# Optimization experiments

Measured on AMD Instinct MI355X. Metric: run time of the kernel, lower is better.

## Reference

```python
import jax, jax.numpy as jnp
import numpy as np

EPS_NORM = 1e-4
EPS_LOG = 1e-6


def normed_weight(W):
    # W: [O, I, K] (K=1). normalize() over dims (1,2) per output channel,
    # with norm scaled by alpha = sqrt(O / (O*I*K)) = 1/sqrt(I*K), then
    # divided again by sqrt(I*K) in get_normed_weight (eval path).
    O, I, K = W.shape
    fan_in = I * K
    norm = jnp.sqrt(jnp.sum(jnp.square(W), axis=(1, 2), keepdims=True))  # [O,1,1]
    norm = EPS_NORM + norm / np.sqrt(fan_in)
    return (W / norm) / np.sqrt(fan_in)


def complex_log(x):
    real = jnp.log(jnp.maximum(jnp.abs(x), EPS_LOG))
    imag = jnp.where(x < 0, jnp.pi, 0.0).astype(real.dtype)
    return jax.lax.complex(real, imag)


def logcumsumexp_complex(z, axis=-1):
    # stable complex logcumsumexp via associative scan:
    # logaddexp(a, b) = m + log(exp(a-m) + exp(b-m)), m = max(Re a, Re b)
    def combine(a, b):
        m = jnp.maximum(a.real, b.real)
        mc = jax.lax.complex(m, jnp.zeros_like(m))
        return mc + jnp.log(jnp.exp(a - mc) + jnp.exp(b - mc))
    return jax.lax.associative_scan(combine, z, axis=axis)


def min_gru(h, g):
    # h, g: [B, C, L]; parallel log-space minGRU recurrence along L
    log_scale = 0.5 * jnp.log(1.0 / jnp.cosh(g) + 1.0)
    log_coeffs = -jax.nn.softplus(g) + log_scale                 # real
    log_values = (-jax.nn.softplus(-g) + log_scale) + complex_log(h)  # complex
    a_star = jnp.cumsum(log_coeffs, axis=-1)                     # real
    a_star_c = jax.lax.complex(a_star, jnp.zeros_like(a_star))
    log_h = a_star_c + logcumsumexp_complex(log_values - a_star_c, axis=-1)
    return jnp.exp(log_h).real


def scaled_cat(xs, axis):
    Ns = [x.shape[axis] for x in xs]
    scale = np.sqrt(np.mean(Ns))
    return scale * jnp.concatenate([x * n ** -0.5 for n, x in zip(Ns, xs)], axis=axis)


def setup_inputs() -> dict:
    key = jax.random.key(0)
    k1, k2 = jax.random.split(key)
    B, D, L = 8, 512, 8192
    x = jax.random.normal(k1, (B, D, L), dtype=jnp.float32)
    W = jax.random.normal(k2, (2 * D, D, 1), dtype=jnp.float32)  # Conv1d(dim, 2*dim, 1) weight
    return {"x": x, "W": W}


def reference(x, W):
    Wn = normed_weight(W)  # [2D, D, 1]
    fb = jnp.einsum('oi,bil->bol', Wn[:, :, 0], x)  # [B, 2D, L]
    fore, back = jnp.split(fb, 2, axis=1)
    h_f, g_f = jnp.split(fore, 2, axis=1)
    back_r = back[..., ::-1]
    h_b, g_b = jnp.split(back_r, 2, axis=1)
    out_f = min_gru(h_f, g_f)
    out_b = min_gru(h_b, g_b)[..., ::-1]
    return scaled_cat([out_f, out_b], axis=1)
```

## Files before the change

kernel.cpp:

```cpp
#include <hip/hip_runtime.h>
#include <math.h>
#include <stdint.h>

#define LSEQ 8192
#define DIN  512
#define NB   8
#define NO   1024

typedef __bf16 bf16x8 __attribute__((ext_vector_type(8)));
typedef float f32x16 __attribute__((ext_vector_type(16)));

__device__ __forceinline__ uint32_t pack_bf16_rne(float lo, float hi) {
    uint32_t ul = __builtin_bit_cast(uint32_t, lo);
    uint32_t uh = __builtin_bit_cast(uint32_t, hi);
    ul += 0x7FFFu + ((ul >> 16) & 1u);
    uh += 0x7FFFu + ((uh >> 16) & 1u);
    return (ul >> 16) | (uh & 0xFFFF0000u);
}
__device__ __forceinline__ float bf16_lo(uint32_t w) {
    return __builtin_bit_cast(float, w << 16);
}
__device__ __forceinline__ float bf16_hi(uint32_t w) {
    return __builtin_bit_cast(float, w & 0xFFFF0000u);
}

__device__ __forceinline__ void gl_lds16(const void* g, void* l) {
    __builtin_amdgcn_global_load_lds(
        (const __attribute__((address_space(1))) void*)g,
        (__attribute__((address_space(3))) void*)l, 16, 0, 0);
}


__global__ void norm_kernel(const float* __restrict__ W, uint32_t* __restrict__ Wnb) {
    const int o = blockIdx.x;
    const int lane = threadIdx.x;
    const float* row = W + (size_t)o * DIN;
    float4 v0 = *(const float4*)(row + lane * 4);
    float4 v1 = *(const float4*)(row + 256 + lane * 4);
    float s = v0.x * v0.x + v0.y * v0.y + v0.z * v0.z + v0.w * v0.w
            + v1.x * v1.x + v1.y * v1.y + v1.z * v1.z + v1.w * v1.w;
#pragma unroll
    for (int m = 32; m; m >>= 1) s += __shfl_xor(s, m, 64);
    const float sq = 22.62741699796952f;
    const float scale = 1.0f / ((1e-4f + sqrtf(s) / sq) * sq);
    uint2 w0, w1;
    w0.x = pack_bf16_rne(v0.x * scale, v0.y * scale);
    w0.y = pack_bf16_rne(v0.z * scale, v0.w * scale);
    w1.x = pack_bf16_rne(v1.x * scale, v1.y * scale);
    w1.y = pack_bf16_rne(v1.z * scale, v1.w * scale);
    const int ot = o >> 7, mb = (o >> 5) & 3, m31 = o & 31;
    const int it0 = lane >> 3;
    const int q   = (lane >> 1) & 3;
    const int wic = (lane & 1) * 2;
    uint32_t* base = Wnb + (size_t)ot * 32768 + ((mb * 4 + q) * 32 + m31) * 4 + wic;
    *(uint2*)&base[(size_t)it0 * 2048] = w0;
    *(uint2*)&base[(size_t)(it0 + 8) * 2048] = w1;
}

__global__ __launch_bounds__(256)
void xpack_kernel(const float* __restrict__ x, uint32_t* __restrict__ xp) {
    __shared__ uint32_t sT[32 * 132];
    const int t  = threadIdx.x;
    const int bx = blockIdx.x;
    const int b  = blockIdx.y;
    const int lt = bx >> 3;
    const int ch = bx & 7;

    const float* xb = x + (size_t)b * DIN * LSEQ + lt * 128;
#pragma unroll
    for (int j = 0; j < 4; ++j) {
        const int idx = j * 256 + t;
        const int k2l = idx >> 5;
        const int lg  = idx & 31;
        const float* r0 = xb + (size_t)(2 * (ch * 32 + k2l)) * LSEQ + lg * 4;
        float4 a = *(const float4*)r0;
        float4 c = *(const float4*)(r0 + LSEQ);
        uint4 wv;
        wv.x = pack_bf16_rne(a.x, c.x);
        wv.y = pack_bf16_rne(a.y, c.y);
        wv.z = pack_bf16_rne(a.z, c.z);
        wv.w = pack_bf16_rne(a.w, c.w);
        *(uint4*)&sT[k2l * 132 + lg * 4] = wv;
    }
    __syncthreads();
    uint32_t* ob = xp + (size_t)(b * 64 + lt) * 32768;
#pragma unroll
    for (int j = 0; j < 4; ++j) {
        const int idx = j * 256 + t;
        const int lp  = idx >> 3;
        const int gq  = idx & 7;
        uint4 wv;
        wv.x = sT[(gq * 4 + 0) * 132 + lp];
        wv.y = sT[(gq * 4 + 1) * 132 + lp];
        wv.z = sT[(gq * 4 + 2) * 132 + lp];
        wv.w = sT[(gq * 4 + 3) * 132 + lp];
        const int itl   = ch * 2 + (gq >> 2);
        const int q     = gq & 3;
        const int chunk = ((lp >> 5) * 4 + q) * 32 + (lp & 31);
        *(uint4*)&ob[(size_t)itl * 2048 + chunk * 4] = wv;
    }
}

__global__ __launch_bounds__(256)
void gemm_kernel(const uint32_t* __restrict__ Wnb, const uint32_t* __restrict__ xp,
                 uint32_t* __restrict__ fbp) {
    __shared__ uint32_t sA[2][2048];
    __shared__ uint32_t sB[2][2048];

    const int tid  = threadIdx.x;
    const int lane = tid & 63;
    const int w    = tid >> 6;
    const int wm   = w & 1, wn = w >> 1;

    const int bx  = blockIdx.x;
    const int xcd = bx & 7;
    const int t   = bx >> 3;
    const int o0t = t & 7;
    const int o0  = o0t * 128;
    const int ltg = xcd + ((t >> 3) << 3);
    const int l0  = ltg * 128;
    const int b   = blockIdx.y;

    const uint32_t* gA = Wnb + (size_t)o0t * 32768 + (w * 2) * 256 + lane * 4;
    const uint32_t* gB = xp + (size_t)(b * 64 + ltg) * 32768 + (w * 2) * 256 + lane * 4;

    f32x16 acc[2][2];
#pragma unroll
    for (int i = 0; i < 2; ++i)
#pragma unroll
        for (int j = 0; j < 2; ++j)
#pragma unroll
            for (int r = 0; r < 16; ++r) acc[i][j][r] = 0.f;

#define STAGE(it, bs)                                               \
    do {                                                            \
        gl_lds16(gA + (size_t)(it) * 2048, &sA[bs][w * 512]);       \
        gl_lds16(gA + (size_t)(it) * 2048 + 256, &sA[bs][w * 512 + 256]); \
        gl_lds16(gB + (size_t)(it) * 2048, &sB[bs][w * 512]);       \
        gl_lds16(gB + (size_t)(it) * 2048 + 256, &sB[bs][w * 512 + 256]); \
    } while (0)

    STAGE(0, 0);
#pragma unroll 2
    for (int it = 0; it < 16; ++it) {
        const int cb = it & 1;
        __syncthreads();
        if (it + 1 < 16) STAGE(it + 1, cb ^ 1);
        const uint32_t* cA = sA[cb];
        const uint32_t* cB = sB[cb];
#pragma unroll
        for (int kh = 0; kh < 2; ++kh) {
            bf16x8 af[2], bfr[2];
#pragma unroll
            for (int ms = 0; ms < 2; ++ms)
                af[ms] = *(const bf16x8*)&cA[((wm * 2 + ms) * 4 + kh * 2) * 128 + lane * 4];
#pragma unroll
            for (int ns = 0; ns < 2; ++ns)
                bfr[ns] = *(const bf16x8*)&cB[((wn * 2 + ns) * 4 + kh * 2) * 128 + lane * 4];
#pragma unroll
            for (int ms = 0; ms < 2; ++ms)
#pragma unroll
                for (int ns = 0; ns < 2; ++ns)
                    acc[ms][ns] = __builtin_amdgcn_mfma_f32_32x32x16_bf16(
                        af[ms], bfr[ns], acc[ms][ns], 0, 0, 0);
        }
    }
#undef STAGE

    uint32_t* fbp_b = fbp + (size_t)b * 512 * LSEQ + l0;
#pragma unroll
    for (int ms = 0; ms < 2; ++ms)
#pragma unroll
        for (int ns = 0; ns < 2; ++ns) {
            const f32x16 a = acc[ms][ns];
            const int rb = o0 + wm * 64 + ms * 32 + 4 * (lane >> 5);
            const int cc = wn * 64 + ns * 32 + (lane & 31);
#pragma unroll
            for (int rp = 0; rp < 8; ++rp) {
                const int r = rp * 2;
                const int row = rb + (r & 3) + 8 * (r >> 2);
                fbp_b[(size_t)(row >> 1) * LSEQ + cc] = pack_bf16_rne(a[r], a[r + 1]);
            }
        }
}

__global__ __launch_bounds__(512)
void scan_kernel(const uint32_t* __restrict__ fbp, float* __restrict__ out) {
    __shared__ uint32_t sbuf[8][2048];
    __shared__ float sA0[8], sB0[8], sA1[8], sB1[8];

    const int bx  = blockIdx.x;
    const int b   = blockIdx.y;
    const int dir = bx >> 7;
    const int p   = bx & 127;
    const int o2h = dir * 256 + p;
    const int o2g = dir * 256 + 128 + p;

    const int t    = threadIdx.x;
    const int lane = t & 63;
    const int w    = t >> 6;

    const uint32_t* hwp = fbp + ((size_t)b * 512 + o2h) * LSEQ + w * 1024;
    const uint32_t* gwp = fbp + ((size_t)b * 512 + o2g) * LSEQ + w * 1024;
    uint32_t* sw = sbuf[w];
    float* swf = (float*)sbuf[w];

#pragma unroll
    for (int i = 0; i < 4; ++i) {
        uint4 v = *(const uint4*)(hwp + i * 256 + lane * 4);
        const uint32_t g = i * 64 + lane;
        const uint32_t gs = g ^ ((g >> 3) & 7);
        *(uint4*)&sw[gs * 4] = v;
    }
#pragma unroll
    for (int i = 0; i < 4; ++i) {
        uint4 v = *(const uint4*)(gwp + i * 256 + lane * 4);
        const uint32_t g = i * 64 + lane;
        const uint32_t gs = g ^ ((g >> 3) & 7);
        *(uint4*)&sw[1024 + gs * 4] = v;
    }
    asm volatile("s_waitcnt lgkmcnt(0)" ::: "memory");

    float av0[16], vv0[16], av1[16], vv1[16];
#pragma unroll
    for (int q = 0; q < 4; ++q) {
        const uint32_t g = lane * 4 + q;
        const uint32_t gs = g ^ ((g >> 3) & 7);
        uint4 hw4 = *(const uint4*)&sw[gs * 4];
        uint4 gw4 = *(const uint4*)&sw[1024 + gs * 4];
        const uint32_t hws[4] = {hw4.x, hw4.y, hw4.z, hw4.w};
        const uint32_t gws[4] = {gw4.x, gw4.y, gw4.z, gw4.w};
#pragma unroll
        for (int s = 0; s < 4; ++s) {
            const int mo = q * 4 + s;
            {
                float g_ = fminf(fmaxf(bf16_lo(gws[s]), -30.f), 30.f);
                float eg = __expf(g_);
                float a  = rsqrtf(fmaf(eg, eg, 1.f));
                float h_ = bf16_lo(hws[s]);
                av0[mo] = a;
                vv0[mo] = a * eg * copysignf(fmaxf(fabsf(h_), 1e-6f), h_);
            }
            {
                float g_ = fminf(fmaxf(bf16_hi(gws[s]), -30.f), 30.f);
                float eg = __expf(g_);
                float a  = rsqrtf(fmaf(eg, eg, 1.f));
                float h_ = bf16_hi(hws[s]);
                av1[mo] = a;
                vv1[mo] = a * eg * copysignf(fmaxf(fabsf(h_), 1e-6f), h_);
            }
        }
    }

    float A0 = 1.f, B0 = 0.f, A1 = 1.f, B1 = 0.f;
    if (dir == 0) {
#pragma unroll
        for (int i = 0; i < 16; ++i) {
            B0 = fmaf(av0[i], B0, vv0[i]); A0 *= av0[i];
            B1 = fmaf(av1[i], B1, vv1[i]); A1 *= av1[i];
        }
    } else {
#pragma unroll
        for (int i = 15; i >= 0; --i) {
            B0 = fmaf(av0[i], B0, vv0[i]); A0 *= av0[i];
            B1 = fmaf(av1[i], B1, vv1[i]); A1 *= av1[i];
        }
    }

    if (dir == 0) {
#pragma unroll
        for (int off = 1; off < 64; off <<= 1) {
            float Ap0 = __shfl_up(A0, (unsigned)off, 64), Bp0 = __shfl_up(B0, (unsigned)off, 64);
            float Ap1 = __shfl_up(A1, (unsigned)off, 64), Bp1 = __shfl_up(B1, (unsigned)off, 64);
            if (lane >= off) {
                B0 = fmaf(A0, Bp0, B0); A0 *= Ap0;
                B1 = fmaf(A1, Bp1, B1); A1 *= Ap1;
            }
        }
        if (lane == 63) { sA0[w] = A0; sB0[w] = B0; sA1[w] = A1; sB1[w] = B1; }
    } else {
#pragma unroll
        for (int off = 1; off < 64; off <<= 1) {
            float Ap0 = __shfl_down(A0, (unsigned)off, 64), Bp0 = __shfl_down(B0, (unsigned)off, 64);
            float Ap1 = __shfl_down(A1, (unsigned)off, 64), Bp1 = __shfl_down(B1, (unsigned)off, 64);
            if (lane + off < 64) {
                B0 = fmaf(A0, Bp0, B0); A0 *= Ap0;
                B1 = fmaf(A1, Bp1, B1); A1 *= Ap1;
            }
        }
        if (lane == 0) { sA0[w] = A0; sB0[w] = B0; sA1[w] = A1; sB1[w] = B1; }
    }
    __syncthreads();
    float WB0 = 0.f, WB1 = 0.f;
    if (dir == 0) {
        for (int wv = 0; wv < w; ++wv) {
            WB0 = fmaf(sA0[wv], WB0, sB0[wv]);
            WB1 = fmaf(sA1[wv], WB1, sB1[wv]);
        }
    } else {
        for (int wv = 7; wv > w; --wv) {
            WB0 = fmaf(sA0[wv], WB0, sB0[wv]);
            WB1 = fmaf(sA1[wv], WB1, sB1[wv]);
        }
    }
    float eA0, eB0, eA1, eB1;
    if (dir == 0) {
        eA0 = __shfl_up(A0, 1u, 64); eB0 = __shfl_up(B0, 1u, 64);
        eA1 = __shfl_up(A1, 1u, 64); eB1 = __shfl_up(B1, 1u, 64);
        if (lane == 0) { eA0 = 1.f; eB0 = 0.f; eA1 = 1.f; eB1 = 0.f; }
    } else {
        eA0 = __shfl_down(A0, 1u, 64); eB0 = __shfl_down(B0, 1u, 64);
        eA1 = __shfl_down(A1, 1u, 64); eB1 = __shfl_down(B1, 1u, 64);
        if (lane == 63) { eA0 = 1.f; eB0 = 0.f; eA1 = 1.f; eB1 = 0.f; }
    }
    float H0 = fmaf(eA0, WB0, eB0);
    float H1 = fmaf(eA1, WB1, eB1);

    if (dir == 0) {
#pragma unroll
        for (int i = 0; i < 16; ++i) {
            H0 = fmaf(av0[i], H0, vv0[i]); vv0[i] = H0;
            H1 = fmaf(av1[i], H1, vv1[i]); vv1[i] = H1;
        }
    } else {
#pragma unroll
        for (int i = 15; i >= 0; --i) {
            H0 = fmaf(av0[i], H0, vv0[i]); vv0[i] = H0;
            H1 = fmaf(av1[i], H1, vv1[i]); vv1[i] = H1;
        }
    }

#pragma unroll
    for (int q = 0; q < 4; ++q) {
        const uint32_t g = lane * 4 + q;
        const uint32_t gs = g ^ ((g >> 3) & 7);
        *(float4*)&swf[gs * 4] =
            make_float4(vv0[q * 4], vv0[q * 4 + 1], vv0[q * 4 + 2], vv0[q * 4 + 3]);
        *(float4*)&swf[1024 + gs * 4] =
            make_float4(vv1[q * 4], vv1[q * 4 + 1], vv1[q * 4 + 2], vv1[q * 4 + 3]);
    }
    asm volatile("s_waitcnt lgkmcnt(0)" ::: "memory");
    const int c0 = 2 * p, c1 = 2 * p + 1;
    float* orow0 = out + ((size_t)b * 512 + dir * 256 + c0) * LSEQ + w * 1024;
    float* orow1 = out + ((size_t)b * 512 + dir * 256 + c1) * LSEQ + w * 1024;
#pragma unroll
    for (int i = 0; i < 4; ++i) {
        const uint32_t g = i * 64 + lane;
        const uint32_t gs = g ^ ((g >> 3) & 7);
        *(float4*)(orow0 + i * 256 + lane * 4) = *(const float4*)&swf[gs * 4];
        *(float4*)(orow1 + i * 256 + lane * 4) = *(const float4*)&swf[1024 + gs * 4];
    }
}

extern "C" void kernel_launch(void* const* d_in, const int* in_sizes, int n_in,
                              void* d_out, int out_size, void* d_ws, size_t ws_size,
                              hipStream_t stream) {
    const float* x = (const float*)d_in[0];
    const float* W = (const float*)d_in[1];
    float* out = (float*)d_out;

    uint32_t* Wnb = (uint32_t*)d_ws;
    uint32_t* fbp = (uint32_t*)((char*)d_ws + (size_t)NO * DIN * 2);
    uint32_t* xp  = (uint32_t*)((char*)d_ws + (size_t)NO * DIN * 2
                                + (size_t)NB * 512 * LSEQ * 4);

    norm_kernel<<<dim3(NO), dim3(64), 0, stream>>>(W, Wnb);
    xpack_kernel<<<dim3(512, NB), dim3(256), 0, stream>>>(x, xp);
    gemm_kernel<<<dim3(512, NB), dim3(256), 0, stream>>>(Wnb, xp, fbp);
    scan_kernel<<<dim3(256, NB), dim3(512), 0, stream>>>(fbp, out);
}
```

Baseline: 350.1 us.

## Deepen GEMM LDS pipeline to four stages with explicit vmcnt waits

The GEMM kernel goes from a two-buffer LDS pipeline to four buffers and prefetches three K-steps ahead. The loop is fully unrolled with explicit s_waitcnt vmcnt counts and raw s_barrier in place of __syncthreads. MFMA issue is wrapped in raised s_setprio. The aim is to hide global-to-LDS load latency better, at the cost of doubling LDS use (64KB per block), which may lower occupancy.

```diff
diff --git a/kernel.cpp b/kernel.cpp
--- a/kernel.cpp
+++ b/kernel.cpp
@@ -104,8 +104,8 @@
 __global__ __launch_bounds__(256)
 void gemm_kernel(const uint32_t* __restrict__ Wnb, const uint32_t* __restrict__ xp,
                  uint32_t* __restrict__ fbp) {
-    __shared__ uint32_t sA[2][2048];
-    __shared__ uint32_t sB[2][2048];
+    __shared__ uint32_t sA[4][2048];
+    __shared__ uint32_t sB[4][2048];
 
     const int tid  = threadIdx.x;
     const int lane = tid & 63;
@@ -132,39 +132,53 @@
 #pragma unroll
             for (int r = 0; r < 16; ++r) acc[i][j][r] = 0.f;
 
-#define STAGE(it, bs)                                               \
-    do {                                                            \
-        gl_lds16(gA + (size_t)(it) * 2048, &sA[bs][w * 512]);       \
-        gl_lds16(gA + (size_t)(it) * 2048 + 256, &sA[bs][w * 512 + 256]); \
-        gl_lds16(gB + (size_t)(it) * 2048, &sB[bs][w * 512]);       \
-        gl_lds16(gB + (size_t)(it) * 2048 + 256, &sB[bs][w * 512 + 256]); \
+#define STAGE(IT, BS)                                                     \
+    do {                                                                  \
+        gl_lds16(gA + (size_t)(IT) * 2048, &sA[BS][w * 512]);             \
+        gl_lds16(gA + (size_t)(IT) * 2048 + 256, &sA[BS][w * 512 + 256]); \
+        gl_lds16(gB + (size_t)(IT) * 2048, &sB[BS][w * 512]);             \
+        gl_lds16(gB + (size_t)(IT) * 2048 + 256, &sB[BS][w * 512 + 256]); \
     } while (0)
 
+#define COMPUTE(CB)                                                                      \
+    do {                                                                                 \
+        _Pragma("unroll") for (int kh = 0; kh < 2; ++kh) {                               \
+            bf16x8 af[2], bfr[2];                                                        \
+            _Pragma("unroll") for (int ms = 0; ms < 2; ++ms)                             \
+                af[ms] = *(const bf16x8*)&sA[CB][((wm * 2 + ms) * 4 + kh * 2) * 128 +    \
+                                                 lane * 4];                              \
+            _Pragma("unroll") for (int ns = 0; ns < 2; ++ns)                             \
+                bfr[ns] = *(const bf16x8*)&sB[CB][((wn * 2 + ns) * 4 + kh * 2) * 128 +   \
+                                                  lane * 4];                             \
+            __builtin_amdgcn_s_setprio(1);                                               \
+            _Pragma("unroll") for (int ms = 0; ms < 2; ++ms)                             \
+                _Pragma("unroll") for (int ns = 0; ns < 2; ++ns)                         \
+                    acc[ms][ns] = __builtin_amdgcn_mfma_f32_32x32x16_bf16(               \
+                        af[ms], bfr[ns], acc[ms][ns], 0, 0, 0);                          \
+            __builtin_amdgcn_s_setprio(0);                                               \
+        }                                                                                \
+    } while (0)
+
+#define STEP(IT, WN)                                             \
+    do {                                                         \
+        asm volatile("s_waitcnt vmcnt(" #WN ")" ::: "memory");   \
+        __builtin_amdgcn_s_barrier();                            \
+        __builtin_amdgcn_sched_barrier(0);                       \
+        if ((IT) + 3 < 16) STAGE((IT) + 3, ((IT) + 3) & 3);      \
+        COMPUTE((IT) & 3);                                       \
+    } while (0)
+
     STAGE(0, 0);
-#pragma unroll 2
-    for (int it = 0; it < 16; ++it) {
-        const int cb = it & 1;
-        __syncthreads();
-        if (it + 1 < 16) STAGE(it + 1, cb ^ 1);
-        const uint32_t* cA = sA[cb];
-        const uint32_t* cB = sB[cb];
-#pragma unroll
-        for (int kh = 0; kh < 2; ++kh) {
-            bf16x8 af[2], bfr[2];
-#pragma unroll
-            for (int ms = 0; ms < 2; ++ms)
-                af[ms] = *(const bf16x8*)&cA[((wm * 2 + ms) * 4 + kh * 2) * 128 + lane * 4];
-#pragma unroll
-            for (int ns = 0; ns < 2; ++ns)
-                bfr[ns] = *(const bf16x8*)&cB[((wn * 2 + ns) * 4 + kh * 2) * 128 + lane * 4];
-#pragma unroll
-            for (int ms = 0; ms < 2; ++ms)
-#pragma unroll
-                for (int ns = 0; ns < 2; ++ns)
-                    acc[ms][ns] = __builtin_amdgcn_mfma_f32_32x32x16_bf16(
-                        af[ms], bfr[ns], acc[ms][ns], 0, 0, 0);
-        }
-    }
+    STAGE(1, 1);
+    STAGE(2, 2);
+    STEP(0, 8);  STEP(1, 8);  STEP(2, 8);  STEP(3, 8);
+    STEP(4, 8);  STEP(5, 8);  STEP(6, 8);  STEP(7, 8);
+    STEP(8, 8);  STEP(9, 8);  STEP(10, 8); STEP(11, 8);
+    STEP(12, 8); STEP(13, 8);
+    STEP(14, 4);
+    STEP(15, 0);
+#undef STEP
+#undef COMPUTE
 #undef STAGE
 
     uint32_t* fbp_b = fbp + (size_t)b * 512 * LSEQ + l0;
```

Result: slower. 362.3 us (+3.5%).

## Drop LDS staging in scan kernel and use 1024 threads with direct vector I/O

Applied to the files above, without the earlier changes.

The scan kernel now runs 1024 threads per block, each owning 8 contiguous timesteps that it loads straight from global memory with two 16-byte loads and writes back with float4 stores. This removes the swizzled shared-memory transpose for both input and output, along with the 16 KB per-wave LDS buffer. The block-level carry combine now spans 16 wavefronts instead of 8. Per-thread global accesses are now strided 32 bytes apart rather than fully coalesced contiguous chunks, and the serial cross-wave prefix loop gets longer.

```diff
diff --git a/kernel.cpp b/kernel.cpp
--- a/kernel.cpp
+++ b/kernel.cpp
@@ -184,10 +184,9 @@
         }
 }
 
-__global__ __launch_bounds__(512)
+__global__ __launch_bounds__(1024)
 void scan_kernel(const uint32_t* __restrict__ fbp, float* __restrict__ out) {
-    __shared__ uint32_t sbuf[8][2048];
-    __shared__ float sA0[8], sB0[8], sA1[8], sB1[8];
+    __shared__ float sA0[16], sB0[16], sA1[16], sB1[16];
 
     const int bx  = blockIdx.x;
     const int b   = blockIdx.y;
@@ -200,54 +199,34 @@
     const int lane = t & 63;
     const int w    = t >> 6;
 
-    const uint32_t* hwp = fbp + ((size_t)b * 512 + o2h) * LSEQ + w * 1024;
-    const uint32_t* gwp = fbp + ((size_t)b * 512 + o2g) * LSEQ + w * 1024;
-    uint32_t* sw = sbuf[w];
-    float* swf = (float*)sbuf[w];
-
-#pragma unroll
-    for (int i = 0; i < 4; ++i) {
-        uint4 v = *(const uint4*)(hwp + i * 256 + lane * 4);
-        const uint32_t g = i * 64 + lane;
-        const uint32_t gs = g ^ ((g >> 3) & 7);
-        *(uint4*)&sw[gs * 4] = v;
-    }
-#pragma unroll
-    for (int i = 0; i < 4; ++i) {
-        uint4 v = *(const uint4*)(gwp + i * 256 + lane * 4);
-        const uint32_t g = i * 64 + lane;
-        const uint32_t gs = g ^ ((g >> 3) & 7);
-        *(uint4*)&sw[1024 + gs * 4] = v;
-    }
-    asm volatile("s_waitcnt lgkmcnt(0)" ::: "memory");
-
-    float av0[16], vv0[16], av1[16], vv1[16];
-#pragma unroll
-    for (int q = 0; q < 4; ++q) {
-        const uint32_t g = lane * 4 + q;
-        const uint32_t gs = g ^ ((g >> 3) & 7);
-        uint4 hw4 = *(const uint4*)&sw[gs * 4];
-        uint4 gw4 = *(const uint4*)&sw[1024 + gs * 4];
-        const uint32_t hws[4] = {hw4.x, hw4.y, hw4.z, hw4.w};
-        const uint32_t gws[4] = {gw4.x, gw4.y, gw4.z, gw4.w};
-#pragma unroll
-        for (int s = 0; s < 4; ++s) {
-            const int mo = q * 4 + s;
+    const uint32_t* hp = fbp + ((size_t)b * 512 + o2h) * LSEQ + t * 8;
+    const uint32_t* gp = fbp + ((size_t)b * 512 + o2g) * LSEQ + t * 8;
+    const uint4 h4a = *(const uint4*)(hp);
+    const uint4 h4b = *(const uint4*)(hp + 4);
+    const uint4 g4a = *(const uint4*)(gp);
+    const uint4 g4b = *(const uint4*)(gp + 4);
+
+    float av0[8], vv0[8], av1[8], vv1[8];
+    {
+        const uint32_t hws[8] = {h4a.x, h4a.y, h4a.z, h4a.w, h4b.x, h4b.y, h4b.z, h4b.w};
+        const uint32_t gws[8] = {g4a.x, g4a.y, g4a.z, g4a.w, g4b.x, g4b.y, g4b.z, g4b.w};
+#pragma unroll
+        for (int s = 0; s < 8; ++s) {
             {
                 float g_ = fminf(fmaxf(bf16_lo(gws[s]), -30.f), 30.f);
                 float eg = __expf(g_);
                 float a  = rsqrtf(fmaf(eg, eg, 1.f));
                 float h_ = bf16_lo(hws[s]);
-                av0[mo] = a;
-                vv0[mo] = a * eg * copysignf(fmaxf(fabsf(h_), 1e-6f), h_);
+                av0[s] = a;
+                vv0[s] = a * eg * copysignf(fmaxf(fabsf(h_), 1e-6f), h_);
             }
             {
                 float g_ = fminf(fmaxf(bf16_hi(gws[s]), -30.f), 30.f);
                 float eg = __expf(g_);
                 float a  = rsqrtf(fmaf(eg, eg, 1.f));
                 float h_ = bf16_hi(hws[s]);
-                av1[mo] = a;
-                vv1[mo] = a * eg * copysignf(fmaxf(fabsf(h_), 1e-6f), h_);
+                av1[s] = a;
+                vv1[s] = a * eg * copysignf(fmaxf(fabsf(h_), 1e-6f), h_);
             }
         }
     }
@@ -255,13 +234,13 @@
     float A0 = 1.f, B0 = 0.f, A1 = 1.f, B1 = 0.f;
     if (dir == 0) {
 #pragma unroll
-        for (int i = 0; i < 16; ++i) {
+        for (int i = 0; i < 8; ++i) {
             B0 = fmaf(av0[i], B0, vv0[i]); A0 *= av0[i];
             B1 = fmaf(av1[i], B1, vv1[i]); A1 *= av1[i];
         }
     } else {
 #pragma unroll
-        for (int i = 15; i >= 0; --i) {
+        for (int i = 7; i >= 0; --i) {
             B0 = fmaf(av0[i], B0, vv0[i]); A0 *= av0[i];
             B1 = fmaf(av1[i], B1, vv1[i]); A1 *= av1[i];
         }
@@ -291,6 +270,7 @@
         if (lane == 0) { sA0[w] = A0; sB0[w] = B0; sA1[w] = A1; sB1[w] = B1; }
     }
     __syncthreads();
+
     float WB0 = 0.f, WB1 = 0.f;
     if (dir == 0) {
         for (int wv = 0; wv < w; ++wv) {
@@ -298,7 +278,7 @@
             WB1 = fmaf(sA1[wv], WB1, sB1[wv]);
         }
     } else {
-        for (int wv = 7; wv > w; --wv) {
+        for (int wv = 15; wv > w; --wv) {
             WB0 = fmaf(sA0[wv], WB0, sB0[wv]);
             WB1 = fmaf(sA1[wv], WB1, sB1[wv]);
         }
@@ -318,38 +298,24 @@
 
     if (dir == 0) {
 #pragma unroll
-        for (int i = 0; i < 16; ++i) {
+        for (int i = 0; i < 8; ++i) {
             H0 = fmaf(av0[i], H0, vv0[i]); vv0[i] = H0;
             H1 = fmaf(av1[i], H1, vv1[i]); vv1[i] = H1;
         }
     } else {
 #pragma unroll
-        for (int i = 15; i >= 0; --i) {
+        for (int i = 7; i >= 0; --i) {
             H0 = fmaf(av0[i], H0, vv0[i]); vv0[i] = H0;
             H1 = fmaf(av1[i], H1, vv1[i]); vv1[i] = H1;
         }
     }
 
-#pragma unroll
-    for (int q = 0; q < 4; ++q) {
-        const uint32_t g = lane * 4 + q;
-        const uint32_t gs = g ^ ((g >> 3) & 7);
-        *(float4*)&swf[gs * 4] =
-            make_float4(vv0[q * 4], vv0[q * 4 + 1], vv0[q * 4 + 2], vv0[q * 4 + 3]);
-        *(float4*)&swf[1024 + gs * 4] =
-            make_float4(vv1[q * 4], vv1[q * 4 + 1], vv1[q * 4 + 2], vv1[q * 4 + 3]);
-    }
-    asm volatile("s_waitcnt lgkmcnt(0)" ::: "memory");
-    const int c0 = 2 * p, c1 = 2 * p + 1;
-    float* orow0 = out + ((size_t)b * 512 + dir * 256 + c0) * LSEQ + w * 1024;
-    float* orow1 = out + ((size_t)b * 512 + dir * 256 + c1) * LSEQ + w * 1024;
-#pragma unroll
-    for (int i = 0; i < 4; ++i) {
-        const uint32_t g = i * 64 + lane;
-        const uint32_t gs = g ^ ((g >> 3) & 7);
-        *(float4*)(orow0 + i * 256 + lane * 4) = *(const float4*)&swf[gs * 4];
-        *(float4*)(orow1 + i * 256 + lane * 4) = *(const float4*)&swf[1024 + gs * 4];
-    }
+    float* orow0 = out + ((size_t)b * 512 + dir * 256 + 2 * p) * LSEQ + t * 8;
+    float* orow1 = orow0 + LSEQ;
+    *(float4*)(orow0)     = make_float4(vv0[0], vv0[1], vv0[2], vv0[3]);
+    *(float4*)(orow0 + 4) = make_float4(vv0[4], vv0[5], vv0[6], vv0[7]);
+    *(float4*)(orow1)     = make_float4(vv1[0], vv1[1], vv1[2], vv1[3]);
+    *(float4*)(orow1 + 4) = make_float4(vv1[4], vv1[5], vv1[6], vv1[7]);
 }
 
 extern "C" void kernel_launch(void* const* d_in, const int* in_sizes, int n_in,
@@ -367,5 +333,5 @@
     norm_kernel<<<dim3(NO), dim3(64), 0, stream>>>(W, Wnb);
     xpack_kernel<<<dim3(512, NB), dim3(256), 0, stream>>>(x, xp);
     gemm_kernel<<<dim3(512, NB), dim3(256), 0, stream>>>(Wnb, xp, fbp);
-    scan_kernel<<<dim3(256, NB), dim3(512), 0, stream>>>(fbp, out);
-}
+    scan_kernel<<<dim3(256, NB), dim3(1024), 0, stream>>>(fbp, out);
+}
```

Measured after the change: 356.3 us. Within noise of the previous version (+1.8%).
